# Performance work log

Measured on AMD Instinct MI355X. Metric: run time of the kernel, lower is better.

Reference implementation:

```python
import jax, jax.numpy as jnp
import numpy as np

EMBED = 1024
HEADS = 16
HEAD_DIM = EMBED // HEADS


def setup_inputs() -> dict:
    key = jax.random.key(0)
    ks = jax.random.split(key, 6)
    scale = 1.0 / np.sqrt(EMBED)
    x = jax.random.normal(ks[0], (2, 2048, EMBED), dtype=jnp.float32)
    # nn.Linear weights stored as [out_features, in_features]
    Wq = jax.random.normal(ks[1], (EMBED, EMBED), dtype=jnp.float32) * scale
    Wk = jax.random.normal(ks[2], (EMBED, EMBED), dtype=jnp.float32) * scale
    Wv = jax.random.normal(ks[3], (EMBED, EMBED), dtype=jnp.float32) * scale
    Wo = jax.random.normal(ks[4], (EMBED, EMBED), dtype=jnp.float32) * scale
    bo = jax.random.normal(ks[5], (EMBED,), dtype=jnp.float32) * scale
    return {"x": x, "Wq": Wq, "Wk": Wk, "Wv": Wv, "Wo": Wo, "bo": bo}


def reference(x, Wq, Wk, Wv, Wo, bo):
    N, L, E = x.shape
    # projections (torch Linear: x @ W.T)
    q = (x @ Wq.T).reshape(N, L, HEADS, HEAD_DIM).transpose(0, 2, 1, 3)  # [N,H,L,D]
    k = (x @ Wk.T).reshape(N, L, HEADS, HEAD_DIM).transpose(0, 2, 1, 3)
    v = (x @ Wv.T).reshape(N, L, HEADS, HEAD_DIM).transpose(0, 2, 1, 3)
    # scores scaled by sqrt(embed_size) (as in source, not sqrt(head_dim))
    scores = jnp.einsum("nhqd,nhkd->nhqk", q, k) / jnp.sqrt(jnp.float32(E))
    attn = jax.nn.softmax(scores, axis=-1)
    out = jnp.einsum("nhqk,nhkd->nhqd", attn, v)  # [N,H,L,D]
    out = out.transpose(0, 2, 1, 3).reshape(N, L, E)
    return out @ Wo.T + bo
```

## Files before the change

kernel.cpp:

```cpp
#include <hip/hip_runtime.h>
#include <hip/hip_bf16.h>

constexpr int NB  = 2;
constexpr int SL  = 2048;
constexpr int EMB = 1024;
constexpr int NH  = 16;
constexpr int HD  = 64;
constexpr int MT  = NB * SL;
constexpr size_t PROJ = (size_t)MT * EMB;

typedef __attribute__((ext_vector_type(8))) short bf16x8;
typedef __attribute__((ext_vector_type(4))) float f32x4;

__device__ inline short f2b(float f) {
  __hip_bfloat16 b = __float2bfloat16(f);
  short s; __builtin_memcpy(&s, &b, 2); return s;
}

#define GLDS16(g, l)                                                     \
  __builtin_amdgcn_global_load_lds(                                      \
      (const __attribute__((address_space(1))) void*)(g),                \
      (__attribute__((address_space(3))) void*)(l), 16, 0, 0)

__global__ __launch_bounds__(256) void cast_all(
    const float* __restrict__ x,  const float* __restrict__ wq,
    const float* __restrict__ wk, const float* __restrict__ wv,
    const float* __restrict__ wo, short* __restrict__ xb,
    short* __restrict__ wqkv, short* __restrict__ wob) {
  const size_t t = (size_t)blockIdx.x * 256 + threadIdx.x;
  const float* src; short* dst; size_t base;
  if (t < 1048576)      { src = x;  dst = xb;              base = 0; }
  else if (t < 1310720) { src = wq; dst = wqkv;            base = 1048576; }
  else if (t < 1572864) { src = wk; dst = wqkv + (1 << 20); base = 1310720; }
  else if (t < 1835008) { src = wv; dst = wqkv + (2 << 20); base = 1572864; }
  else                  { src = wo; dst = wob;             base = 1835008; }
  const size_t i = t - base;
  const float4 v = ((const float4*)src)[i];
  const short4 o = {f2b(v.x), f2b(v.y), f2b(v.z), f2b(v.w)};
  ((short4*)dst)[i] = o;
}

__global__ __launch_bounds__(256) void gemm_qkv(
    const short* __restrict__ A, const short* __restrict__ W,
    short* __restrict__ qb, short* __restrict__ kb, short* __restrict__ vt) {
  __shared__ short As[128 * 32];
  __shared__ short Bs[128 * 32];
  const int tid = threadIdx.x;
  const int w = tid >> 6, lane = tid & 63;
  const int la = lane >> 4, lb = lane & 15;
  const int wm = w & 1, wn = w >> 1;
  const int m0 = blockIdx.y << 7, n0 = blockIdx.x << 7;
  const int srow = lane >> 2, scol = (lane & 3) << 3;
  const short* a0 = A + (size_t)(m0 + w * 16 + srow) * 1024 + scol;
  const short* b0 = W + (size_t)(n0 + w * 16 + srow) * 1024 + scol;
  short* lA0 = As + (w * 16) * 32;
  short* lA1 = As + (64 + w * 16) * 32;
  short* lB0 = Bs + (w * 16) * 32;
  short* lB1 = Bs + (64 + w * 16) * 32;

  f32x4 acc[4][4];
#pragma unroll
  for (int i = 0; i < 4; ++i)
#pragma unroll
    for (int j = 0; j < 4; ++j) acc[i][j] = (f32x4){0.f, 0.f, 0.f, 0.f};

  for (int k0 = 0; k0 < 1024; k0 += 32) {
    __syncthreads();
    GLDS16(a0 + k0, lA0);
    GLDS16(a0 + 64 * 1024 + k0, lA1);
    GLDS16(b0 + k0, lB0);
    GLDS16(b0 + 64 * 1024 + k0, lB1);
    __syncthreads();
    bf16x8 af[4], bf[4];
#pragma unroll
    for (int i = 0; i < 4; ++i)
      af[i] = *(const bf16x8*)&As[(wm * 64 + i * 16 + lb) * 32 + la * 8];
#pragma unroll
    for (int j = 0; j < 4; ++j)
      bf[j] = *(const bf16x8*)&Bs[(wn * 64 + j * 16 + lb) * 32 + la * 8];
#pragma unroll
    for (int i = 0; i < 4; ++i)
#pragma unroll
      for (int j = 0; j < 4; ++j)
        acc[i][j] = __builtin_amdgcn_mfma_f32_16x16x32_bf16(af[i], bf[j],
                                                            acc[i][j], 0, 0, 0);
  }

  const int region = n0 >> 10;
  if (region < 2) {
    short* dst = region ? kb : qb;
    const float sc = region ? 1.0f : 0.03125f * 1.44269504f;
    const int nb0 = n0 & 1023;
#pragma unroll
    for (int j = 0; j < 4; ++j) {
      const int nj = nb0 + wn * 64 + j * 16 + lb;
#pragma unroll
      for (int i = 0; i < 4; ++i) {
        const int mi = m0 + wm * 64 + i * 16 + la * 4;
#pragma unroll
        for (int r = 0; r < 4; ++r)
          dst[(size_t)(mi + r) * 1024 + nj] = f2b(acc[i][j][r] * sc);
      }
    }
  } else {
#pragma unroll
    for (int j = 0; j < 4; ++j) {
      const int nv = (n0 - 2048) + wn * 64 + j * 16 + lb;
      const int h = nv >> 6, d = nv & 63;
#pragma unroll
      for (int i = 0; i < 4; ++i) {
        const int mi = m0 + wm * 64 + i * 16 + la * 4;
        const int nbi = mi >> 11, seq = mi & (SL - 1);
        const int k5 = seq & 31;
        const int seqp = (seq & ~31) | (8 * ((k5 >> 2) & 3) + 4 * (k5 >> 4));
        const short4 o = {f2b(acc[i][j][0]), f2b(acc[i][j][1]),
                          f2b(acc[i][j][2]), f2b(acc[i][j][3])};
        *(short4*)&vt[((size_t)(nbi * NH + h) * HD + d) * SL + seqp] = o;
      }
    }
  }
}

__global__ __launch_bounds__(256) void gemm_out(
    const short* __restrict__ A, const short* __restrict__ W,
    const float* __restrict__ bias, float* __restrict__ out) {
  __shared__ short As[128 * 32];
  __shared__ short Bs[64 * 32];
  const int tid = threadIdx.x;
  const int w = tid >> 6, lane = tid & 63;
  const int la = lane >> 4, lb = lane & 15;
  const int wm = w & 1, wn = w >> 1;
  const int m0 = blockIdx.y << 7, n0 = blockIdx.x << 6;
  const int srow = lane >> 2, scol = (lane & 3) << 3;
  const short* a0 = A + (size_t)(m0 + w * 16 + srow) * 1024 + scol;
  const short* b0 = W + (size_t)(n0 + w * 16 + srow) * 1024 + scol;
  short* lA0 = As + (w * 16) * 32;
  short* lA1 = As + (64 + w * 16) * 32;
  short* lB0 = Bs + (w * 16) * 32;

  f32x4 acc[4][2];
#pragma unroll
  for (int i = 0; i < 4; ++i)
#pragma unroll
    for (int j = 0; j < 2; ++j) acc[i][j] = (f32x4){0.f, 0.f, 0.f, 0.f};

  for (int k0 = 0; k0 < 1024; k0 += 32) {
    __syncthreads();
    GLDS16(a0 + k0, lA0);
    GLDS16(a0 + 64 * 1024 + k0, lA1);
    GLDS16(b0 + k0, lB0);
    __syncthreads();
    bf16x8 af[4], bf[2];
#pragma unroll
    for (int i = 0; i < 4; ++i)
      af[i] = *(const bf16x8*)&As[(wm * 64 + i * 16 + lb) * 32 + la * 8];
#pragma unroll
    for (int j = 0; j < 2; ++j)
      bf[j] = *(const bf16x8*)&Bs[(wn * 32 + j * 16 + lb) * 32 + la * 8];
#pragma unroll
    for (int i = 0; i < 4; ++i)
#pragma unroll
      for (int j = 0; j < 2; ++j)
        acc[i][j] = __builtin_amdgcn_mfma_f32_16x16x32_bf16(af[i], bf[j],
                                                            acc[i][j], 0, 0, 0);
  }
#pragma unroll
  for (int j = 0; j < 2; ++j) {
    const int nj = n0 + wn * 32 + j * 16 + lb;
    const float bv = bias[nj];
#pragma unroll
    for (int i = 0; i < 4; ++i) {
      const int mi = m0 + wm * 64 + i * 16 + la * 4;
#pragma unroll
      for (int r = 0; r < 4; ++r)
        out[(size_t)(mi + r) * 1024 + nj] = acc[i][j][r] + bv;
    }
  }
}

__global__ __launch_bounds__(256, 2) void attn_mfma(const short* __restrict__ Qg,
                                                    const short* __restrict__ Kg,
                                                    const short* __restrict__ Vtg,
                                                    short* __restrict__ Ab) {
  __shared__ __align__(16) short smem[2 * 17920];
  __shared__ float lred[128];
  const int tid = threadIdx.x;
  const int w = tid >> 6, lane = tid & 63;
  const int G = lane >> 4, lb = lane & 15;
  const int wk = w & 1, wq = w >> 1;
  const int h = blockIdx.x, qt = blockIdx.y, n = blockIdx.z;
  const int krow = tid >> 3, kcol = (tid & 7) << 3;
  const int vrow = tid >> 4, vcol = (tid & 15) << 3;

  const short* Qb = Qg + ((size_t)(n * SL + (qt << 7) + 64 * wq)) * EMB + h * HD;
  bf16x8 bQ[4][2];
#pragma unroll
  for (int nt = 0; nt < 4; ++nt)
#pragma unroll
    for (int ks = 0; ks < 2; ++ks)
      bQ[nt][ks] =
          *(const bf16x8*)(Qb + (size_t)(16 * nt + lb) * EMB + 32 * ks + 8 * G);

  f32x4 O[4][4];
  float lacc[4] = {0.f, 0.f, 0.f, 0.f};
#pragma unroll
  for (int i = 0; i < 4; ++i)
#pragma unroll
    for (int j = 0; j < 4; ++j) O[i][j] = (f32x4){0.f, 0.f, 0.f, 0.f};

  const short* Kb0 = Kg + ((size_t)(n * SL)) * EMB + h * HD;
  const short* Vb0 = Vtg + ((size_t)(n * NH + h)) * HD * SL;

  bf16x8 pk[4], pv[4];
#pragma unroll
  for (int k = 0; k < 4; ++k)
    pk[k] = *(const bf16x8*)(Kb0 + (size_t)(krow + 32 * k) * EMB + kcol);
#pragma unroll
  for (int r = 0; r < 4; ++r)
    pv[r] = *(const bf16x8*)(Vb0 + (size_t)(vrow + 16 * r) * SL + vcol);

  for (int kt = 0; kt < SL / 128; ++kt) {
    short* Ks = &smem[(kt & 1) * 17920];
    short* Vt = Ks + 128 * 72;
#pragma unroll
    for (int k = 0; k < 4; ++k)
      *(bf16x8*)&Ks[(krow + 32 * k) * 72 + kcol] = pk[k];
#pragma unroll
    for (int r = 0; r < 4; ++r)
      *(bf16x8*)&Vt[(vrow + 16 * r) * 136 + vcol] = pv[r];
    __syncthreads();

    if (kt + 1 < SL / 128) {
      const short* Kb = Kb0 + (size_t)(kt + 1) * 128 * EMB;
#pragma unroll
      for (int k = 0; k < 4; ++k)
        pk[k] = *(const bf16x8*)(Kb + (size_t)(krow + 32 * k) * EMB + kcol);
#pragma unroll
      for (int r = 0; r < 4; ++r)
        pv[r] = *(const bf16x8*)(Vb0 + (size_t)(vrow + 16 * r) * SL +
                                 (kt + 1) * 128 + vcol);
    }

#pragma unroll
    for (int s = 0; s < 2; ++s) {
      const int kb = 64 * wk + 32 * s;
      f32x4 S[2][4];
#pragma unroll
      for (int mt = 0; mt < 2; ++mt)
#pragma unroll
        for (int nt = 0; nt < 4; ++nt) S[mt][nt] = (f32x4){0.f, 0.f, 0.f, 0.f};
#pragma unroll
      for (int ks = 0; ks < 2; ++ks) {
        const bf16x8 aK0 = *(const bf16x8*)&Ks[(kb + lb) * 72 + 32 * ks + 8 * G];
        const bf16x8 aK1 =
            *(const bf16x8*)&Ks[(kb + 16 + lb) * 72 + 32 * ks + 8 * G];
#pragma unroll
        for (int nt = 0; nt < 4; ++nt) {
          S[0][nt] = __builtin_amdgcn_mfma_f32_16x16x32_bf16(aK0, bQ[nt][ks],
                                                             S[0][nt], 0, 0, 0);
          S[1][nt] = __builtin_amdgcn_mfma_f32_16x16x32_bf16(aK1, bQ[nt][ks],
                                                             S[1][nt], 0, 0, 0);
        }
      }

#pragma unroll
      for (int nt = 0; nt < 4; ++nt)
#pragma unroll
        for (int mt = 0; mt < 2; ++mt)
#pragma unroll
          for (int r = 0; r < 4; ++r) {
            const float p = __builtin_amdgcn_exp2f(S[mt][nt][r]);
            S[mt][nt][r] = p;
            lacc[nt] += p;
          }

      bf16x8 aV[4];
#pragma unroll
      for (int mtd = 0; mtd < 4; ++mtd)
        aV[mtd] = *(const bf16x8*)&Vt[(16 * mtd + lb) * 136 + kb + 8 * G];
#pragma unroll
      for (int nt = 0; nt < 4; ++nt) {
        bf16x8 B2;
        B2[0] = f2b(S[0][nt][0]);
        B2[1] = f2b(S[0][nt][1]);
        B2[2] = f2b(S[0][nt][2]);
        B2[3] = f2b(S[0][nt][3]);
        B2[4] = f2b(S[1][nt][0]);
        B2[5] = f2b(S[1][nt][1]);
        B2[6] = f2b(S[1][nt][2]);
        B2[7] = f2b(S[1][nt][3]);
#pragma unroll
        for (int mtd = 0; mtd < 4; ++mtd)
          O[mtd][nt] = __builtin_amdgcn_mfma_f32_16x16x32_bf16(aV[mtd], B2,
                                                               O[mtd][nt], 0, 0, 0);
      }
    }
  }

#pragma unroll
  for (int nt = 0; nt < 4; ++nt) {
    lacc[nt] += __shfl_xor(lacc[nt], 16);
    lacc[nt] += __shfl_xor(lacc[nt], 32);
  }

  float* red = (float*)smem;
  __syncthreads();
  if (wk == 1) {
#pragma unroll
    for (int nt = 0; nt < 4; ++nt) {
      const int q = 16 * nt + lb;
#pragma unroll
      for (int mtd = 0; mtd < 4; ++mtd)
        *(f32x4*)&red[wq * 4352 + q * 68 + 16 * mtd + 4 * G] = O[mtd][nt];
      if (G == 0) lred[wq * 64 + q] = lacc[nt];
    }
  }
  __syncthreads();
  if (wk == 0) {
    short* Ao = Ab + ((size_t)(n * SL + (qt << 7) + 64 * wq)) * EMB + h * HD;
#pragma unroll
    for (int nt = 0; nt < 4; ++nt) {
      const int q = 16 * nt + lb;
      const float inv = 1.f / (lacc[nt] + lred[wq * 64 + q]);
#pragma unroll
      for (int mtd = 0; mtd < 4; ++mtd) {
        const f32x4 t = *(const f32x4*)&red[wq * 4352 + q * 68 + 16 * mtd + 4 * G];
        const f32x4 s = t + O[mtd][nt];
        const short4 o = {f2b(s[0] * inv), f2b(s[1] * inv), f2b(s[2] * inv),
                          f2b(s[3] * inv)};
        *(short4*)(Ao + (size_t)q * EMB + 16 * mtd + 4 * G) = o;
      }
    }
  }
}

extern "C" void kernel_launch(void* const* d_in, const int* in_sizes, int n_in,
                              void* d_out, int out_size, void* d_ws, size_t ws_size,
                              hipStream_t stream) {
  const float* x  = (const float*)d_in[0];
  const float* Wq = (const float*)d_in[1];
  const float* Wk = (const float*)d_in[2];
  const float* Wv = (const float*)d_in[3];
  const float* Wo = (const float*)d_in[4];
  const float* bo = (const float*)d_in[5];
  float* out = (float*)d_out;

  short* xb   = (short*)d_ws;
  short* wqkv = xb + PROJ;
  short* wob  = wqkv + 3u * EMB * EMB;
  short* qb   = wob + (size_t)EMB * EMB;
  short* kb   = qb + PROJ;
  short* vt   = kb + PROJ;
  short* ab   = qb;

  cast_all<<<8192, 256, 0, stream>>>(x, Wq, Wk, Wv, Wo, xb, wqkv, wob);
  gemm_qkv<<<dim3(24, 32), 256, 0, stream>>>(xb, wqkv, qb, kb, vt);
  attn_mfma<<<dim3(NH, SL / 128, NB), 256, 0, stream>>>(qb, kb, vt, ab);
  gemm_out<<<dim3(16, 32), 256, 0, stream>>>(ab, wob, bo, out);
}
```

Measured before the change: 178.3 us.

## Pre-swizzle K and V into MFMA fragment order and load directly to registers

The QKV projection epilogue now writes K and V in a per-head layout that matches the MFMA operand fragments, so each lane reads its operand with one contiguous 16-byte global load. The attention kernel no longer stages K/V through double-buffered shared memory and drops the per-tile barriers. Each wave streams its own key blocks with register double-buffering. This removes LDS traffic and synchronisation, at the cost of more register pressure and scattered 2-byte writes in the projection epilogue for K.

Result: no change. 175.5 us (-1.6%).

```diff
diff --git a/kernel.cpp b/kernel.cpp
--- a/kernel.cpp
+++ b/kernel.cpp
@@ -71,51 +71,67 @@
     GLDS16(b0 + k0, lB0);
     GLDS16(b0 + 64 * 1024 + k0, lB1);
     __syncthreads();
-    bf16x8 af[4], bf[4];
+    bf16x8 af[4], bfr[4];
 #pragma unroll
     for (int i = 0; i < 4; ++i)
       af[i] = *(const bf16x8*)&As[(wm * 64 + i * 16 + lb) * 32 + la * 8];
 #pragma unroll
     for (int j = 0; j < 4; ++j)
-      bf[j] = *(const bf16x8*)&Bs[(wn * 64 + j * 16 + lb) * 32 + la * 8];
+      bfr[j] = *(const bf16x8*)&Bs[(wn * 64 + j * 16 + lb) * 32 + la * 8];
 #pragma unroll
     for (int i = 0; i < 4; ++i)
 #pragma unroll
       for (int j = 0; j < 4; ++j)
-        acc[i][j] = __builtin_amdgcn_mfma_f32_16x16x32_bf16(af[i], bf[j],
+        acc[i][j] = __builtin_amdgcn_mfma_f32_16x16x32_bf16(af[i], bfr[j],
                                                             acc[i][j], 0, 0, 0);
   }
 
   const int region = n0 >> 10;
-  if (region < 2) {
-    short* dst = region ? kb : qb;
-    const float sc = region ? 1.0f : 0.03125f * 1.44269504f;
-    const int nb0 = n0 & 1023;
+  if (region == 0) {
+    const float sc = 0.03125f * 1.44269504f;
 #pragma unroll
     for (int j = 0; j < 4; ++j) {
-      const int nj = nb0 + wn * 64 + j * 16 + lb;
+      const int nj = (n0 & 1023) + wn * 64 + j * 16 + lb;
 #pragma unroll
       for (int i = 0; i < 4; ++i) {
         const int mi = m0 + wm * 64 + i * 16 + la * 4;
 #pragma unroll
         for (int r = 0; r < 4; ++r)
-          dst[(size_t)(mi + r) * 1024 + nj] = f2b(acc[i][j][r] * sc);
+          qb[(size_t)(mi + r) * 1024 + nj] = f2b(acc[i][j][r] * sc);
       }
     }
-  } else {
+  } else if (region == 1) {
 #pragma unroll
     for (int j = 0; j < 4; ++j) {
-      const int nv = (n0 - 2048) + wn * 64 + j * 16 + lb;
-      const int h = nv >> 6, d = nv & 63;
+      const int nj = (n0 & 1023) + wn * 64 + j * 16 + lb;
+      const int hh = nj >> 6, d = nj & 63;
+      const int ks = d >> 5, Gd = (d >> 3) & 3, jj = d & 7;
 #pragma unroll
       for (int i = 0; i < 4; ++i) {
         const int mi = m0 + wm * 64 + i * 16 + la * 4;
         const int nbi = mi >> 11, seq = mi & (SL - 1);
-        const int k5 = seq & 31;
-        const int seqp = (seq & ~31) | (8 * ((k5 >> 2) & 3) + 4 * (k5 >> 4));
+        const size_t base = ((size_t)(nbi * NH + hh) << 17) +
+                            (size_t)(seq >> 4) * 1024 + ks * 512 + Gd * 128 +
+                            (seq & 15) * 8 + jj;
+#pragma unroll
+        for (int r = 0; r < 4; ++r) kb[base + r * 8] = f2b(acc[i][j][r]);
+      }
+    }
+  } else {
+#pragma unroll
+    for (int j = 0; j < 4; ++j) {
+      const int nv = (n0 - 2048) + wn * 64 + j * 16 + lb;
+      const int hh = nv >> 6, d = nv & 63;
+      const int mtd = d >> 4, lbv = d & 15;
+#pragma unroll
+      for (int i = 0; i < 4; ++i) {
+        const int mi = m0 + wm * 64 + i * 16 + la * 4;
+        const int nbi = mi >> 11, seq = mi & (SL - 1);
+        const int kq = seq >> 5, g = (seq >> 2) & 3, hi = (seq >> 4) & 1;
         const short4 o = {f2b(acc[i][j][0]), f2b(acc[i][j][1]),
                           f2b(acc[i][j][2]), f2b(acc[i][j][3])};
-        *(short4*)&vt[((size_t)(nbi * NH + h) * HD + d) * SL + seqp] = o;
+        *(short4*)&vt[((size_t)(nbi * NH + hh) << 17) + (size_t)kq * 2048 +
+                      mtd * 512 + g * 128 + lbv * 8 + 4 * hi] = o;
       }
     }
   }
@@ -150,18 +166,18 @@
     GLDS16(a0 + 64 * 1024 + k0, lA1);
     GLDS16(b0 + k0, lB0);
     __syncthreads();
-    bf16x8 af[4], bf[2];
+    bf16x8 af[4], bfr[2];
 #pragma unroll
     for (int i = 0; i < 4; ++i)
       af[i] = *(const bf16x8*)&As[(wm * 64 + i * 16 + lb) * 32 + la * 8];
 #pragma unroll
     for (int j = 0; j < 2; ++j)
-      bf[j] = *(const bf16x8*)&Bs[(wn * 32 + j * 16 + lb) * 32 + la * 8];
+      bfr[j] = *(const bf16x8*)&Bs[(wn * 32 + j * 16 + lb) * 32 + la * 8];
 #pragma unroll
     for (int i = 0; i < 4; ++i)
 #pragma unroll
       for (int j = 0; j < 2; ++j)
-        acc[i][j] = __builtin_amdgcn_mfma_f32_16x16x32_bf16(af[i], bf[j],
+        acc[i][j] = __builtin_amdgcn_mfma_f32_16x16x32_bf16(af[i], bfr[j],
                                                             acc[i][j], 0, 0, 0);
   }
 #pragma unroll
@@ -178,19 +194,62 @@
   }
 }
 
+#define LOADK(DK, KB32)                                                      \
+  do {                                                                       \
+    _Pragma("unroll") for (int rr_ = 0; rr_ < 2; ++rr_)                      \
+        _Pragma("unroll") for (int ks_ = 0; ks_ < 2; ++ks_)                  \
+            DK[rr_][ks_] = *(const bf16x8*)(Kb + (size_t)(KB32) * 2048 +     \
+                                            rr_ * 1024 + ks_ * 512);         \
+  } while (0)
+
+#define LOADV(DV, KB32)                                                      \
+  do {                                                                       \
+    _Pragma("unroll") for (int md_ = 0; md_ < 4; ++md_)                      \
+        DV[md_] = *(const bf16x8*)(Vb + (size_t)(KB32) * 2048 + md_ * 512);  \
+  } while (0)
+
+#define ATTN_STEP(AK, AV)                                                    \
+  do {                                                                       \
+    f32x4 S[2][4];                                                           \
+    _Pragma("unroll") for (int mt = 0; mt < 2; ++mt)                         \
+        _Pragma("unroll") for (int nt = 0; nt < 4; ++nt)                     \
+            S[mt][nt] = (f32x4){0.f, 0.f, 0.f, 0.f};                         \
+    _Pragma("unroll") for (int ks = 0; ks < 2; ++ks)                         \
+        _Pragma("unroll") for (int nt = 0; nt < 4; ++nt) {                   \
+      S[0][nt] = __builtin_amdgcn_mfma_f32_16x16x32_bf16(AK[0][ks],          \
+                     bQ[nt][ks], S[0][nt], 0, 0, 0);                         \
+      S[1][nt] = __builtin_amdgcn_mfma_f32_16x16x32_bf16(AK[1][ks],          \
+                     bQ[nt][ks], S[1][nt], 0, 0, 0);                         \
+    }                                                                        \
+    _Pragma("unroll") for (int nt = 0; nt < 4; ++nt) {                       \
+      _Pragma("unroll") for (int mt = 0; mt < 2; ++mt)                       \
+          _Pragma("unroll") for (int r = 0; r < 4; ++r) {                    \
+        const float p = __builtin_amdgcn_exp2f(S[mt][nt][r]);                \
+        S[mt][nt][r] = p;                                                    \
+        lacc[nt] += p;                                                       \
+      }                                                                      \
+      bf16x8 B2;                                                             \
+      B2[0] = f2b(S[0][nt][0]); B2[1] = f2b(S[0][nt][1]);                    \
+      B2[2] = f2b(S[0][nt][2]); B2[3] = f2b(S[0][nt][3]);                    \
+      B2[4] = f2b(S[1][nt][0]); B2[5] = f2b(S[1][nt][1]);                    \
+      B2[6] = f2b(S[1][nt][2]); B2[7] = f2b(S[1][nt][3]);                    \
+      _Pragma("unroll") for (int mtd = 0; mtd < 4; ++mtd)                    \
+          O[mtd][nt] = __builtin_amdgcn_mfma_f32_16x16x32_bf16(              \
+              AV[mtd], B2, O[mtd][nt], 0, 0, 0);                             \
+    }                                                                        \
+  } while (0)
+
 __global__ __launch_bounds__(256, 2) void attn_mfma(const short* __restrict__ Qg,
-                                                    const short* __restrict__ Kg,
-                                                    const short* __restrict__ Vtg,
+                                                    const short* __restrict__ Kp,
+                                                    const short* __restrict__ Vp,
                                                     short* __restrict__ Ab) {
-  __shared__ __align__(16) short smem[2 * 17920];
+  __shared__ __align__(16) float red[2][64][68];
   __shared__ float lred[128];
   const int tid = threadIdx.x;
   const int w = tid >> 6, lane = tid & 63;
   const int G = lane >> 4, lb = lane & 15;
   const int wk = w & 1, wq = w >> 1;
   const int h = blockIdx.x, qt = blockIdx.y, n = blockIdx.z;
-  const int krow = tid >> 3, kcol = (tid & 7) << 3;
-  const int vrow = tid >> 4, vcol = (tid & 15) << 3;
 
   const short* Qb = Qg + ((size_t)(n * SL + (qt << 7) + 64 * wq)) * EMB + h * HD;
   bf16x8 bQ[4][2];
@@ -208,93 +267,22 @@
 #pragma unroll
     for (int j = 0; j < 4; ++j) O[i][j] = (f32x4){0.f, 0.f, 0.f, 0.f};
 
-  const short* Kb0 = Kg + ((size_t)(n * SL)) * EMB + h * HD;
-  const short* Vb0 = Vtg + ((size_t)(n * NH + h)) * HD * SL;
-
-  bf16x8 pk[4], pv[4];
-#pragma unroll
-  for (int k = 0; k < 4; ++k)
-    pk[k] = *(const bf16x8*)(Kb0 + (size_t)(krow + 32 * k) * EMB + kcol);
-#pragma unroll
-  for (int r = 0; r < 4; ++r)
-    pv[r] = *(const bf16x8*)(Vb0 + (size_t)(vrow + 16 * r) * SL + vcol);
-
-  for (int kt = 0; kt < SL / 128; ++kt) {
-    short* Ks = &smem[(kt & 1) * 17920];
-    short* Vt = Ks + 128 * 72;
-#pragma unroll
-    for (int k = 0; k < 4; ++k)
-      *(bf16x8*)&Ks[(krow + 32 * k) * 72 + kcol] = pk[k];
-#pragma unroll
-    for (int r = 0; r < 4; ++r)
-      *(bf16x8*)&Vt[(vrow + 16 * r) * 136 + vcol] = pv[r];
-    __syncthreads();
-
-    if (kt + 1 < SL / 128) {
-      const short* Kb = Kb0 + (size_t)(kt + 1) * 128 * EMB;
-#pragma unroll
-      for (int k = 0; k < 4; ++k)
-        pk[k] = *(const bf16x8*)(Kb + (size_t)(krow + 32 * k) * EMB + kcol);
-#pragma unroll
-      for (int r = 0; r < 4; ++r)
-        pv[r] = *(const bf16x8*)(Vb0 + (size_t)(vrow + 16 * r) * SL +
-                                 (kt + 1) * 128 + vcol);
-    }
-
-#pragma unroll
-    for (int s = 0; s < 2; ++s) {
-      const int kb = 64 * wk + 32 * s;
-      f32x4 S[2][4];
-#pragma unroll
-      for (int mt = 0; mt < 2; ++mt)
-#pragma unroll
-        for (int nt = 0; nt < 4; ++nt) S[mt][nt] = (f32x4){0.f, 0.f, 0.f, 0.f};
-#pragma unroll
-      for (int ks = 0; ks < 2; ++ks) {
-        const bf16x8 aK0 = *(const bf16x8*)&Ks[(kb + lb) * 72 + 32 * ks + 8 * G];
-        const bf16x8 aK1 =
-            *(const bf16x8*)&Ks[(kb + 16 + lb) * 72 + 32 * ks + 8 * G];
-#pragma unroll
-        for (int nt = 0; nt < 4; ++nt) {
-          S[0][nt] = __builtin_amdgcn_mfma_f32_16x16x32_bf16(aK0, bQ[nt][ks],
-                                                             S[0][nt], 0, 0, 0);
-          S[1][nt] = __builtin_amdgcn_mfma_f32_16x16x32_bf16(aK1, bQ[nt][ks],
-                                                             S[1][nt], 0, 0, 0);
-        }
-      }
-
-#pragma unroll
-      for (int nt = 0; nt < 4; ++nt)
-#pragma unroll
-        for (int mt = 0; mt < 2; ++mt)
-#pragma unroll
-          for (int r = 0; r < 4; ++r) {
-            const float p = __builtin_amdgcn_exp2f(S[mt][nt][r]);
-            S[mt][nt][r] = p;
-            lacc[nt] += p;
-          }
-
-      bf16x8 aV[4];
-#pragma unroll
-      for (int mtd = 0; mtd < 4; ++mtd)
-        aV[mtd] = *(const bf16x8*)&Vt[(16 * mtd + lb) * 136 + kb + 8 * G];
-#pragma unroll
-      for (int nt = 0; nt < 4; ++nt) {
-        bf16x8 B2;
-        B2[0] = f2b(S[0][nt][0]);
-        B2[1] = f2b(S[0][nt][1]);
-        B2[2] = f2b(S[0][nt][2]);
-        B2[3] = f2b(S[0][nt][3]);
-        B2[4] = f2b(S[1][nt][0]);
-        B2[5] = f2b(S[1][nt][1]);
-        B2[6] = f2b(S[1][nt][2]);
-        B2[7] = f2b(S[1][nt][3]);
-#pragma unroll
-        for (int mtd = 0; mtd < 4; ++mtd)
-          O[mtd][nt] = __builtin_amdgcn_mfma_f32_16x16x32_bf16(aV[mtd], B2,
-                                                               O[mtd][nt], 0, 0, 0);
-      }
-    }
+  const short* Kb = Kp + (((size_t)(n * NH + h)) << 17) + lane * 8;
+  const short* Vb = Vp + (((size_t)(n * NH + h)) << 17) + lane * 8;
+
+  bf16x8 K0[2][2], V0[4], K1[2][2], V1[4];
+  LOADK(K0, 2 * wk);
+  LOADV(V0, 2 * wk);
+  for (int it = 0; it < 32; it += 2) {
+    const int kA = 2 * it + 2 * wk;
+    LOADK(K1, kA + 1);
+    LOADV(V1, kA + 1);
+    ATTN_STEP(K0, V0);
+    if (it + 2 < 32) {
+      LOADK(K0, kA + 4);
+      LOADV(V0, kA + 4);
+    }
+    ATTN_STEP(K1, V1);
   }
 
 #pragma unroll
@@ -303,15 +291,13 @@
     lacc[nt] += __shfl_xor(lacc[nt], 32);
   }
 
-  float* red = (float*)smem;
-  __syncthreads();
   if (wk == 1) {
 #pragma unroll
     for (int nt = 0; nt < 4; ++nt) {
       const int q = 16 * nt + lb;
 #pragma unroll
       for (int mtd = 0; mtd < 4; ++mtd)
-        *(f32x4*)&red[wq * 4352 + q * 68 + 16 * mtd + 4 * G] = O[mtd][nt];
+        *(f32x4*)&red[wq][q][16 * mtd + 4 * G] = O[mtd][nt];
       if (G == 0) lred[wq * 64 + q] = lacc[nt];
     }
   }
@@ -324,7 +310,7 @@
       const float inv = 1.f / (lacc[nt] + lred[wq * 64 + q]);
 #pragma unroll
       for (int mtd = 0; mtd < 4; ++mtd) {
-        const f32x4 t = *(const f32x4*)&red[wq * 4352 + q * 68 + 16 * mtd + 4 * G];
+        const f32x4 t = *(const f32x4*)&red[wq][q][16 * mtd + 4 * G];
         const f32x4 s = t + O[mtd][nt];
         const short4 o = {f2b(s[0] * inv), f2b(s[1] * inv), f2b(s[2] * inv),
                           f2b(s[3] * inv)};
```
